# Optimization experiments

Measured on AMD Instinct MI355X. Metric: run time of the kernel, lower is better.

Reference implementation:

```python
import jax, jax.numpy as jnp
import numpy as np

D_MODEL = 1024
N_HEADS = 16
D_HEAD = D_MODEL // N_HEADS
FF = 4 * D_MODEL
B, S = 1, 2048
ROPE_BASE = 10000.0
LN_EPS = 1e-5


def setup_inputs() -> dict:
    key = jax.random.key(0)
    ks = jax.random.split(key, 12)
    sd = 0.02
    return {
        "x": jax.random.normal(ks[0], (B, S, D_MODEL), dtype=jnp.float32),
        # weights stored [in, out]
        "w_qkv": jax.random.normal(ks[1], (D_MODEL, 3 * D_MODEL), dtype=jnp.float32) * sd,
        "w_attn": jax.random.normal(ks[2], (D_MODEL, D_MODEL), dtype=jnp.float32) * sd,
        "b_attn": jnp.zeros((D_MODEL,), dtype=jnp.float32),
        "w_ff1": jax.random.normal(ks[3], (D_MODEL, FF), dtype=jnp.float32) * sd,
        "b_ff1": jnp.zeros((FF,), dtype=jnp.float32),
        "w_ff2": jax.random.normal(ks[4], (FF, D_MODEL), dtype=jnp.float32) * sd,
        "b_ff2": jnp.zeros((D_MODEL,), dtype=jnp.float32),
        "ln1_g": jnp.ones((D_MODEL,), dtype=jnp.float32),
        "ln1_b": jnp.zeros((D_MODEL,), dtype=jnp.float32),
        "ln2_g": jnp.ones((D_MODEL,), dtype=jnp.float32),
        "ln2_b": jnp.zeros((D_MODEL,), dtype=jnp.float32),
    }


def _layernorm(x, g, b):
    mu = jnp.mean(x, axis=-1, keepdims=True)
    var = jnp.mean(jnp.square(x - mu), axis=-1, keepdims=True)
    return (x - mu) * jax.lax.rsqrt(var + LN_EPS) * g + b


def _rope_cos_sin(seq_len, d_head, dtype):
    # scale=1.0 -> dynamic YaRN degenerates to vanilla RoPE with mscale=1
    inv_freq = 1.0 / (ROPE_BASE ** (jnp.arange(0, d_head, 2, dtype=jnp.float32) / d_head))
    pos = jnp.arange(seq_len, dtype=jnp.float32)
    freqs = pos[:, None] * inv_freq[None, :]          # [S, D/2]
    emb = jnp.concatenate([freqs, freqs], axis=-1)    # [S, D]
    return jnp.cos(emb).astype(dtype), jnp.sin(emb).astype(dtype)


def _rotate_half(x):
    x1, x2 = jnp.split(x, 2, axis=-1)
    return jnp.concatenate([-x2, x1], axis=-1)


def _apply_rope(q, k, cos, sin):
    # q,k: [B,S,H,D]; cos/sin: [S,D]
    c = cos[None, :, None, :]
    s = sin[None, :, None, :]
    return q * c + _rotate_half(q) * s, k * c + _rotate_half(k) * s


def _block(x, w_qkv, w_attn, b_attn, w_ff1, b_ff1, w_ff2, b_ff2,
           ln1_g, ln1_b, ln2_g, ln2_b):
    b, s, d = x.shape
    # --- attention sub-block (pre-norm) ---
    h = _layernorm(x, ln1_g, ln1_b)
    qkv = h @ w_qkv                                   # [B,S,3D]
    xq, xk, xv = jnp.split(qkv, 3, axis=-1)
    xq = xq.reshape(b, s, N_HEADS, D_HEAD)
    xk = xk.reshape(b, s, N_HEADS, D_HEAD)
    xv = xv.reshape(b, s, N_HEADS, D_HEAD)
    cos, sin = _rope_cos_sin(s, D_HEAD, x.dtype)
    xq, xk = _apply_rope(xq, xk, cos, sin)
    scale = 1.0 / np.sqrt(D_HEAD)
    scores = jnp.einsum("bqhd,bkhd->bhqk", xq, xk) * scale
    causal = jnp.tril(jnp.ones((s, s), dtype=bool))
    scores = jnp.where(causal[None, None], scores, jnp.finfo(scores.dtype).min)
    probs = jax.nn.softmax(scores, axis=-1)
    att = jnp.einsum("bhqk,bkhd->bqhd", probs, xv).reshape(b, s, d)
    x = x + (att @ w_attn + b_attn)
    # --- feed-forward sub-block (pre-norm) ---
    h2 = _layernorm(x, ln2_g, ln2_b)
    ff = jax.nn.gelu(h2 @ w_ff1 + b_ff1, approximate=False) @ w_ff2 + b_ff2
    return x + ff


def reference(x, w_qkv, w_attn, b_attn, w_ff1, b_ff1, w_ff2, b_ff2,
              ln1_g, ln1_b, ln2_g, ln2_b):
    return _block(x, w_qkv, w_attn, b_attn, w_ff1, b_ff1, w_ff2, b_ff2,
                  ln1_g, ln1_b, ln2_g, ln2_b)
```

## Files before the change

### kernel.cpp

```cpp
#include <hip/hip_runtime.h>
#include <hip/hip_bf16.h>
#include <stdint.h>

#define DM   1024
#define SEQ  2048
#define NH   16
#define DH   64
#define FFD  4096

typedef float  f32x4  __attribute__((ext_vector_type(4)));
typedef float  f32x16 __attribute__((ext_vector_type(16)));
typedef __bf16 bf16x8 __attribute__((ext_vector_type(8)));
typedef unsigned short u16;
typedef unsigned short u16x4v __attribute__((ext_vector_type(4)));
typedef unsigned short u16x8 __attribute__((ext_vector_type(8)));

__device__ __forceinline__ u16 f2bf(float f){
    unsigned int u = __builtin_bit_cast(unsigned int, f);
    u = u + 0x7FFFu + ((u >> 16) & 1u);
    return (u16)(u >> 16);
}
__device__ __forceinline__ float bf2f(u16 v){
    unsigned int u = ((unsigned int)v) << 16;
    return __builtin_bit_cast(float, u);
}
__device__ __forceinline__ f32x4 zero4(){ f32x4 v; v[0]=0.f;v[1]=0.f;v[2]=0.f;v[3]=0.f; return v; }
__device__ __forceinline__ unsigned int cvtpk(float lo, float hi){
    unsigned int r;
    asm("v_cvt_pk_bf16_f32 %0, %1, %2" : "=v"(r) : "v"(lo), "v"(hi));
    return r;
}

__device__ __forceinline__ void gload_lds16(const void* g, void* l){
    __builtin_amdgcn_global_load_lds(
        (const __attribute__((address_space(1))) unsigned int*)(uintptr_t)g,
        (__attribute__((address_space(3))) unsigned int*)(uintptr_t)l,
        16, 0, 0);
}

__global__ __launch_bounds__(256) void transall_k(const float* __restrict__ s0, u16* __restrict__ d0,
                                                  const float* __restrict__ s1, u16* __restrict__ d1,
                                                  const float* __restrict__ s2, u16* __restrict__ d2,
                                                  const float* __restrict__ s3, u16* __restrict__ d3){
    __shared__ float tile[64][65];
    const int b = blockIdx.x;
    const float* src; u16* dst; int K, N, bx, by;
    if (b < 768)      { src = s0; dst = d0; K = 1024; N = 3072; bx = b % 48;          by = b / 48; }
    else if (b < 1024){ src = s1; dst = d1; K = 1024; N = 1024; bx = (b-768) % 16;    by = (b-768) / 16; }
    else if (b < 2048){ src = s2; dst = d2; K = 1024; N = 4096; bx = (b-1024) % 64;   by = (b-1024) / 64; }
    else              { src = s3; dst = d3; K = 4096; N = 1024; bx = (b-2048) % 16;   by = (b-2048) / 16; }
    const int n0 = bx * 64, k0 = by * 64;
    const int t = threadIdx.x;
#pragma unroll
    for (int i = 0; i < 16; ++i){
        int idx = t + i * 256;
        int r = idx >> 6, c = idx & 63;
        tile[r][c] = src[(size_t)(k0 + r) * N + n0 + c];
    }
    __syncthreads();
#pragma unroll
    for (int i = 0; i < 16; ++i){
        int idx = t + i * 256;
        int r = idx >> 6, c = idx & 63;
        dst[(size_t)(n0 + r) * K + k0 + c] = f2bf(tile[c][r]);
    }
}

__global__ __launch_bounds__(256) void ln_k(const float* __restrict__ in,
                                            const float* __restrict__ gw,
                                            const float* __restrict__ bw,
                                            u16* __restrict__ out){
    const int row = blockIdx.x, t = threadIdx.x;
    f32x4 vv = *((const f32x4*)(in + (size_t)row * DM) + t);
    float v[4];
#pragma unroll
    for (int j = 0; j < 4; ++j) v[j] = vv[j];
    float s = 0.f, ss = 0.f;
#pragma unroll
    for (int j = 0; j < 4; ++j){ s += v[j]; ss += v[j] * v[j]; }
#pragma unroll
    for (int off = 1; off < 64; off <<= 1){
        s  += __shfl_xor(s,  off, 64);
        ss += __shfl_xor(ss, off, 64);
    }
    __shared__ float rs_[4], rss_[4];
    const int w = t >> 6;
    if ((t & 63) == 0){ rs_[w] = s; rss_[w] = ss; }
    __syncthreads();
    s  = rs_[0] + rs_[1] + rs_[2] + rs_[3];
    ss = rss_[0] + rss_[1] + rss_[2] + rss_[3];
    const float mean = s * (1.f / DM);
    const float var  = ss * (1.f / DM) - mean * mean;
    const float rstd = rsqrtf(var + 1e-5f);
#pragma unroll
    for (int j = 0; j < 4; ++j){
        int c = t * 4 + j;
        out[(size_t)row * DM + c] = f2bf((v[j] - mean) * rstd * gw[c] + bw[c]);
    }
}

template<int TM, int TN, int WR, int WC, int EPI>
__global__ __launch_bounds__(256) void gemm_k(const u16* __restrict__ A,
                                              const u16* __restrict__ Bt,
                                              const float* __restrict__ bias,
                                              const float* __restrict__ resid,
                                              void* __restrict__ out,
                                              u16* __restrict__ qout,
                                              u16* __restrict__ kout,
                                              u16* __restrict__ vout,
                                              int M, int N, int K){
    constexpr int MR   = TM / WR / 16;
    constexpr int NR   = TN / WC / 16;
    constexpr int AISS = (TM * 64) / 4096;
    constexpr int BISS = (TN * 64) / 4096;
    __shared__ u16 ldsAll[2 * TM * 32 + 2 * TN * 32];
    u16* ldsA = ldsAll;
    u16* ldsB = ldsAll + 2 * TM * 32;
    const int t = threadIdx.x;
    const int L = t & 63, w = t >> 6;
    const int g = L >> 4, li = L & 15;
    const int wr = w / WC, wc = w % WC;
    const int rowbase = wr * (TM / WR);
    const int colbase = wc * (TN / WC);
    const int nxb  = M / TM;
    const int nper = (int)gridDim.x >> 3;
    const int jswz = ((int)blockIdx.x & 7) * nper + ((int)blockIdx.x >> 3);
    const int brow = (jswz % nxb) * TM, bcol = (jswz / nxb) * TN;

    const u16* aPtr = A  + (size_t)brow * K;
    const u16* bPtr = Bt + (size_t)bcol * K;

    f32x4 acc[MR][NR];
#pragma unroll
    for (int m = 0; m < MR; ++m)
#pragma unroll
        for (int n = 0; n < NR; ++n) acc[m][n] = zero4();

    auto STAGE = [&](int buf, int ko){
#pragma unroll
        for (int i = 0; i < AISS; ++i){
            int o = i * 256 + t;
            gload_lds16(aPtr + (size_t)(o >> 2) * K + (o & 3) * 8 + ko, &ldsA[buf * TM * 32 + o * 8]);
        }
#pragma unroll
        for (int i = 0; i < BISS; ++i){
            int o = i * 256 + t;
            gload_lds16(bPtr + (size_t)(o >> 2) * K + (o & 3) * 8 + ko, &ldsB[buf * TN * 32 + o * 8]);
        }
    };

    const int KT = K >> 5;
    int cur = 0;
    STAGE(0, 0);
    __syncthreads();
    for (int kt = 0; kt < KT; ++kt){
        if (kt + 1 < KT) STAGE(cur ^ 1, (kt + 1) * 32);
        bf16x8 af[MR], bfr[NR];
#pragma unroll
        for (int m = 0; m < MR; ++m)
            af[m]  = *(const bf16x8*)&ldsA[cur * TM * 32 + (rowbase + m * 16 + li) * 32 + g * 8];
#pragma unroll
        for (int n = 0; n < NR; ++n)
            bfr[n] = *(const bf16x8*)&ldsB[cur * TN * 32 + (colbase + n * 16 + li) * 32 + g * 8];
#pragma unroll
        for (int m = 0; m < MR; ++m)
#pragma unroll
            for (int n = 0; n < NR; ++n)
                acc[m][n] = __builtin_amdgcn_mfma_f32_16x16x32_bf16(af[m], bfr[n], acc[m][n], 0, 0, 0);
        __syncthreads();
        cur ^= 1;
    }

    if constexpr (EPI == 4){
        const int colabs = bcol + colbase;
        const int part = colabs >> 10;
        if (part < 2){
            u16* dst = (part == 0) ? qout : kout;
            const int h = (colabs >> 6) & 15;
            float freq[2];
#pragma unroll
            for (int n = 0; n < 2; ++n)
                freq[n] = powf(10000.f, -(float)(n * 16 + li) * (1.f / 32.f));
#pragma unroll
            for (int m = 0; m < MR; ++m)
#pragma unroll
                for (int r = 0; r < 4; ++r){
                    const int srow = brow + rowbase + m * 16 + g * 4 + r;
                    const size_t tb = (size_t)(h * 64 + (srow >> 5)) * 2048
                                    + (li >> 3) * 256 + (srow & 31) * 8 + (li & 7);
#pragma unroll
                    for (int n = 0; n < 2; ++n){
                        float lo = acc[m][n][r], hi = acc[m][n + 2][r];
                        float sn, cs;
                        sincosf((float)srow * freq[n], &sn, &cs);
                        dst[tb + n * 512]       = f2bf(lo * cs - hi * sn);
                        dst[tb + (n + 2) * 512] = f2bf(hi * cs + lo * sn);
                    }
                }
        } else {
            u16* tileT = ldsAll;
            __syncthreads();
#pragma unroll
            for (int m = 0; m < MR; ++m)
#pragma unroll
                for (int n = 0; n < NR; ++n)
#pragma unroll
                    for (int r = 0; r < 4; ++r){
                        const int row = rowbase + m * 16 + g * 4 + r;
                        const int col = colbase + n * 16 + li;
                        tileT[col * 72 + row] = f2bf(acc[m][n][r]);
                    }
            __syncthreads();
            const int dv = t >> 1, half = t & 1;
            const int habs = ((bcol + dv) >> 6) & 15;
            const int dvl = dv & 63;
            const int f = dvl >> 5, dv5 = dvl & 31;
            const int tt = (brow >> 5) + half;
            u16* vbase = vout + (size_t)(habs * 64 + tt) * 2048 + f * 256 + dv5 * 8;
#pragma unroll
            for (int j = 0; j < 4; ++j)
                *(u16x8*)(vbase + (j >> 1) * 1024 + (j & 1) * 512)
                    = *(const u16x8*)&tileT[dv * 72 + half * 32 + j * 8];
        }
        return;
    }

#pragma unroll
    for (int m = 0; m < MR; ++m)
#pragma unroll
        for (int n = 0; n < NR; ++n)
#pragma unroll
            for (int r = 0; r < 4; ++r){
                const int row = brow + rowbase + m * 16 + g * 4 + r;
                const int col = bcol + colbase + n * 16 + li;
                float v = acc[m][n][r];
                if constexpr (EPI == 1){
                    v += bias[col] + resid[(size_t)row * N + col];
                    ((float*)out)[(size_t)row * N + col] = v;
                } else if constexpr (EPI == 2){
                    v += bias[col];
                    v = 0.5f * v * (1.f + erff(v * 0.70710678f));
                    ((u16*)out)[(size_t)row * N + col] = f2bf(v);
                } else {
                    v += bias[col] + resid[(size_t)row * N + col];
                    ((float*)out)[(size_t)row * N + col] = v;
                }
            }
}

#define CHT 8
__global__ __launch_bounds__(256) void attn_k(const u16* __restrict__ Qh,
                                              const u16* __restrict__ Kh,
                                              const u16* __restrict__ VT,
                                              u16* __restrict__ Opart,
                                              float* __restrict__ ml){
    const int t = threadIdx.x, w = t >> 6, L = t & 63;
    const int bid = blockIdx.x;
    const int xcd = bid & 7;
    const int lj  = (bid >> 3) * 4 + w;
    const int h   = xcd * 2 + (lj & 1);
    const int jd  = lj >> 1;
    int g = 7, rem = jd;
    while (rem >= 8 * (g + 1)){ rem -= 8 * (g + 1); --g; }
    const int gp1 = g + 1;
    const int qt = 8 * g + 7 - rem / gp1;
    const int c  = rem % gp1;
    const int t0 = c * CHT;
    const int tEnd = min(t0 + CHT, qt + 1);
    const int l31 = L & 31, H = L >> 5;

    const size_t hT = (size_t)h * 64;
    const int lane_off = H * 256 + l31 * 8;
    const int vlane_off = H * 512 + l31 * 8;

    const u16* qB = Qh + (hT + qt) * 2048 + lane_off;
    bf16x8 qf0 = *(const bf16x8*)(qB);
    bf16x8 qf1 = *(const bf16x8*)(qB + 512);
    bf16x8 qf2 = *(const bf16x8*)(qB + 1024);
    bf16x8 qf3 = *(const bf16x8*)(qB + 1536);

    const u16* kB0 = Kh + (hT + t0) * 2048 + lane_off;
    bf16x8 kc0 = *(const bf16x8*)(kB0);
    bf16x8 kc1 = *(const bf16x8*)(kB0 + 512);
    bf16x8 kc2 = *(const bf16x8*)(kB0 + 1024);
    bf16x8 kc3 = *(const bf16x8*)(kB0 + 1536);

    f32x16 O0, O1;
#pragma unroll
    for (int i = 0; i < 16; ++i){ O0[i] = 0.f; O1[i] = 0.f; }
    float m = -3.0e4f, lsum = 0.f;

    for (int tt = t0; tt < tEnd; ++tt){
        const u16* vB = VT + (hT + tt) * 2048 + vlane_off;
        bf16x8 v00 = *(const bf16x8*)(vB);
        bf16x8 v01 = *(const bf16x8*)(vB + 1024);
        bf16x8 v10 = *(const bf16x8*)(vB + 256);
        bf16x8 v11 = *(const bf16x8*)(vB + 1280);

        f32x16 st;
#pragma unroll
        for (int i = 0; i < 16; ++i) st[i] = 0.f;
        st = __builtin_amdgcn_mfma_f32_32x32x16_bf16(kc0, qf0, st, 0, 0, 0);
        st = __builtin_amdgcn_mfma_f32_32x32x16_bf16(kc1, qf1, st, 0, 0, 0);
        st = __builtin_amdgcn_mfma_f32_32x32x16_bf16(kc2, qf2, st, 0, 0, 0);
        st = __builtin_amdgcn_mfma_f32_32x32x16_bf16(kc3, qf3, st, 0, 0, 0);

        const bool more = (tt + 1 < tEnd);
        bf16x8 kn0, kn1, kn2, kn3;
        if (more){
            const u16* kBn = Kh + (hT + tt + 1) * 2048 + lane_off;
            kn0 = *(const bf16x8*)(kBn);
            kn1 = *(const bf16x8*)(kBn + 512);
            kn2 = *(const bf16x8*)(kBn + 1024);
            kn3 = *(const bf16x8*)(kBn + 1536);
        }

        const bool diag = (tt == qt);
        float sv[16];
#pragma unroll
        for (int i = 0; i < 16; ++i){
            float x = st[i] * 0.125f;
            if (diag){
                int kkl = (i & 3) + 8 * (i >> 2) + 4 * H;
                if (kkl > l31) x = -3.0e4f;
            }
            sv[i] = x;
        }
        float smax = sv[0];
#pragma unroll
        for (int i = 1; i < 16; ++i) smax = fmaxf(smax, sv[i]);
        smax = fmaxf(smax, __shfl_xor(smax, 32, 64));
        const float nm = fmaxf(m, smax);
        const float alpha = __expf(m - nm);
        m = nm;
        float ps = 0.f;
#pragma unroll
        for (int i = 0; i < 16; ++i){ sv[i] = __expf(sv[i] - m); ps += sv[i]; }
        ps += __shfl_xor(ps, 32, 64);
        lsum = lsum * alpha + ps;
#pragma unroll
        for (int i = 0; i < 16; ++i){ O0[i] *= alpha; O1[i] *= alpha; }

        unsigned int A0 = cvtpk(sv[0],  sv[1]),  A1 = cvtpk(sv[2],  sv[3]);
        unsigned int B0 = cvtpk(sv[4],  sv[5]),  B1 = cvtpk(sv[6],  sv[7]);
        unsigned int C0 = cvtpk(sv[8],  sv[9]),  C1 = cvtpk(sv[10], sv[11]);
        unsigned int D0 = cvtpk(sv[12], sv[13]), D1 = cvtpk(sv[14], sv[15]);
        unsigned int eA0 = (unsigned int)__shfl_xor((int)A0, 32, 64);
        unsigned int eA1 = (unsigned int)__shfl_xor((int)A1, 32, 64);
        unsigned int eB0 = (unsigned int)__shfl_xor((int)B0, 32, 64);
        unsigned int eB1 = (unsigned int)__shfl_xor((int)B1, 32, 64);
        unsigned int eC0 = (unsigned int)__shfl_xor((int)C0, 32, 64);
        unsigned int eC1 = (unsigned int)__shfl_xor((int)C1, 32, 64);
        unsigned int eD0 = (unsigned int)__shfl_xor((int)D0, 32, 64);
        unsigned int eD1 = (unsigned int)__shfl_xor((int)D1, 32, 64);
        union Uw { unsigned int w[4]; bf16x8 v; };
        Uw f0, f1;
        f0.w[0] = H ? eB0 : A0;  f0.w[1] = H ? eB1 : A1;
        f0.w[2] = H ? B0  : eA0; f0.w[3] = H ? B1  : eA1;
        f1.w[0] = H ? eD0 : C0;  f1.w[1] = H ? eD1 : C1;
        f1.w[2] = H ? D0  : eC0; f1.w[3] = H ? D1  : eC1;

        O0 = __builtin_amdgcn_mfma_f32_32x32x16_bf16(v00, f0.v, O0, 0, 0, 0);
        O0 = __builtin_amdgcn_mfma_f32_32x32x16_bf16(v01, f1.v, O0, 0, 0, 0);
        O1 = __builtin_amdgcn_mfma_f32_32x32x16_bf16(v10, f0.v, O1, 0, 0, 0);
        O1 = __builtin_amdgcn_mfma_f32_32x32x16_bf16(v11, f1.v, O1, 0, 0, 0);

        if (more){ kc0 = kn0; kc1 = kn1; kc2 = kn2; kc3 = kn3; }
    }

    const int jobd = h * 288 + jd;
    const size_t ob = (size_t)jobd * (32 * 64);
    const int q = l31;
#pragma unroll
    for (int f = 0; f < 2; ++f){
        const int dv0 = f * 32;
#pragma unroll
        for (int k = 0; k < 4; ++k){
            u16x4v pkv;
#pragma unroll
            for (int e = 0; e < 4; ++e)
                pkv[e] = f2bf(f == 0 ? O0[k * 4 + e] : O1[k * 4 + e]);
            *(u16x4v*)(Opart + ob + (size_t)q * 64 + dv0 + 8 * k + 4 * H) = pkv;
        }
    }
    if (H == 0){
        ml[((size_t)jobd * 32 + q) * 2]     = m;
        ml[((size_t)jobd * 32 + q) * 2 + 1] = lsum;
    }
}

__global__ __launch_bounds__(256) void combine_k(const u16* __restrict__ Opart,
                                                 const float* __restrict__ ml,
                                                 u16* __restrict__ att){
    const int qt = blockIdx.x, h = blockIdx.y;
    const int g = qt >> 3, gp1 = g + 1;
    const int off = 8 * (36 - ((gp1 * (g + 2)) >> 1));
    const int jd0 = off + (8 * g + 7 - qt) * gp1;
    const int j0 = h * 288 + jd0;
    const int nact = gp1;
    const int t = threadIdx.x;
    const int q = t >> 3, dv0 = (t & 7) * 8;

    float m = -3.0e30f;
    for (int cc = 0; cc < nact; ++cc)
        m = fmaxf(m, ml[((size_t)(j0 + cc) * 32 + q) * 2]);
    float Ls = 0.f;
    float o[8];
#pragma unroll
    for (int j = 0; j < 8; ++j) o[j] = 0.f;
    for (int cc = 0; cc < nact; ++cc){
        const float mv = ml[((size_t)(j0 + cc) * 32 + q) * 2];
        const float lv = ml[((size_t)(j0 + cc) * 32 + q) * 2 + 1];
        const float wgt = __expf(mv - m);
        Ls += wgt * lv;
        const u16* src = Opart + ((size_t)(j0 + cc) * 32 + q) * 64 + dv0;
        u16x8 a = *(const u16x8*)src;
#pragma unroll
        for (int e = 0; e < 8; ++e) o[e] += wgt * bf2f(a[e]);
    }
    const float inv = 1.f / Ls;
    const int qg = qt * 32 + q;
#pragma unroll
    for (int j = 0; j < 8; ++j)
        att[(size_t)qg * DM + h * 64 + dv0 + j] = f2bf(o[j] * inv);
}

extern "C" void kernel_launch(void* const* d_in, const int* in_sizes, int n_in,
                              void* d_out, int out_size, void* d_ws, size_t ws_size,
                              hipStream_t stream){
    (void)in_sizes; (void)n_in; (void)out_size; (void)ws_size;
    const float* x      = (const float*)d_in[0];
    const float* w_qkv  = (const float*)d_in[1];
    const float* w_attn = (const float*)d_in[2];
    const float* b_attn = (const float*)d_in[3];
    const float* w_ff1  = (const float*)d_in[4];
    const float* b_ff1  = (const float*)d_in[5];
    const float* w_ff2  = (const float*)d_in[6];
    const float* b_ff2  = (const float*)d_in[7];
    const float* ln1g   = (const float*)d_in[8];
    const float* ln1b   = (const float*)d_in[9];
    const float* ln2g   = (const float*)d_in[10];
    const float* ln2b   = (const float*)d_in[11];

    char* ws = (char*)d_ws;
    const size_t MB = 1u << 20;
    u16*   T1    = (u16*)(ws + 0);
    u16*   T2    = (u16*)(ws + 6  * MB);
    u16*   T3    = (u16*)(ws + 8  * MB);
    u16*   T4    = (u16*)(ws + 16 * MB);
    u16*   h1    = (u16*)(ws + 24 * MB);
    u16*   Qh    = (u16*)(ws + 28 * MB);
    u16*   Kh    = (u16*)(ws + 32 * MB);
    u16*   VT    = (u16*)(ws + 36 * MB);
    u16*   Opart = (u16*)(ws + 40 * MB);
    float* mlbuf = (float*)(ws + 59 * MB);
    u16*   att   = (u16*)(ws + 0);
    float* x2    = (float*)(ws + 40 * MB);
    u16*   h2    = (u16*)(ws + 4  * MB);
    u16*   ff    = (u16*)(ws + 24 * MB);

    transall_k<<<3072, 256, 0, stream>>>(w_qkv, T1, w_attn, T2, w_ff1, T3, w_ff2, T4);
    ln_k<<<SEQ, 256, 0, stream>>>(x, ln1g, ln1b, h1);
    gemm_k<64,128,2,2,4><<<768, 256, 0, stream>>>(h1, T1, nullptr, nullptr, nullptr,
                                                  Qh, Kh, VT, SEQ, 3072, 1024);
    attn_k<<<1152, 256, 0, stream>>>(Qh, Kh, VT, Opart, mlbuf);
    combine_k<<<dim3(64, 16), 256, 0, stream>>>(Opart, mlbuf, att);
    gemm_k<64,64,2,2,1><<<512, 256, 0, stream>>>(att, T2, b_attn, x, x2,
                                                 nullptr, nullptr, nullptr, SEQ, 1024, 1024);
    ln_k<<<SEQ, 256, 0, stream>>>(x2, ln2g, ln2b, h2);
    gemm_k<64,128,1,4,2><<<1024, 256, 0, stream>>>(h2, T3, b_ff1, nullptr, ff,
                                                   nullptr, nullptr, nullptr, SEQ, 4096, 1024);
    gemm_k<64,64,2,2,3><<<512, 256, 0, stream>>>(ff, T4, b_ff2, x2, (float*)d_out,
                                                 nullptr, nullptr, nullptr, SEQ, 1024, 4096);
}
```

Baseline: 178.4 us.

## Split-K the attention-output and FF2 GEMMs with a separate reduction kernel

Adds an NS split-K template parameter to the GEMM kernel. Each block computes a K-chunk and writes fp32 partials, and a new gcomb_k kernel sums them and adds the bias and residual. The attention-output GEMM uses 2 splits and the FF2 GEMM uses 4, which multiplies block counts to improve CU occupancy and shorten each block's long K loop. In exchange it adds extra global traffic for the partial buffers (up to 32 MB for FF2) and two extra kernel launches. It also assumes the workspace can hold the partials starting at 48 MB.

```diff
diff --git a/kernel.cpp b/kernel.cpp
--- a/kernel.cpp
+++ b/kernel.cpp
@@ -99,7 +99,7 @@
     }
 }
 
-template<int TM, int TN, int WR, int WC, int EPI>
+template<int TM, int TN, int WR, int WC, int EPI, int NS = 1>
 __global__ __launch_bounds__(256) void gemm_k(const u16* __restrict__ A,
                                               const u16* __restrict__ Bt,
                                               const float* __restrict__ bias,
@@ -123,12 +123,17 @@
     const int rowbase = wr * (TM / WR);
     const int colbase = wc * (TN / WC);
     const int nxb  = M / TM;
+    const int nyb  = N / TN;
     const int nper = (int)gridDim.x >> 3;
     const int jswz = ((int)blockIdx.x & 7) * nper + ((int)blockIdx.x >> 3);
-    const int brow = (jswz % nxb) * TM, bcol = (jswz / nxb) * TN;
-
-    const u16* aPtr = A  + (size_t)brow * K;
-    const u16* bPtr = Bt + (size_t)bcol * K;
+    int j2 = jswz, chunk = 0;
+    if (NS > 1){ chunk = j2 / (nxb * nyb); j2 -= chunk * (nxb * nyb); }
+    const int brow = (j2 % nxb) * TM, bcol = (j2 / nxb) * TN;
+    const int KC = K / NS;
+    const int kb = chunk * KC;
+
+    const u16* aPtr = A  + (size_t)brow * K + kb;
+    const u16* bPtr = Bt + (size_t)bcol * K + kb;
 
     f32x4 acc[MR][NR];
 #pragma unroll
@@ -149,7 +154,7 @@
         }
     };
 
-    const int KT = K >> 5;
+    const int KT = KC >> 5;
     int cur = 0;
     STAGE(0, 0);
     __syncthreads();
@@ -234,7 +239,9 @@
                 const int row = brow + rowbase + m * 16 + g * 4 + r;
                 const int col = bcol + colbase + n * 16 + li;
                 float v = acc[m][n][r];
-                if constexpr (EPI == 1){
+                if constexpr (NS > 1){
+                    ((float*)out)[((size_t)chunk * M + row) * N + col] = v;
+                } else if constexpr (EPI == 1){
                     v += bias[col] + resid[(size_t)row * N + col];
                     ((float*)out)[(size_t)row * N + col] = v;
                 } else if constexpr (EPI == 2){
@@ -246,6 +253,27 @@
                     ((float*)out)[(size_t)row * N + col] = v;
                 }
             }
+}
+
+template<int NS>
+__global__ __launch_bounds__(256) void gcomb_k(const float* __restrict__ P,
+                                               const float* __restrict__ bias,
+                                               const float* __restrict__ resid,
+                                               float* __restrict__ out){
+    const size_t base = ((size_t)blockIdx.x * 256 + threadIdx.x) * 4;
+    const int col = (int)(base & 1023);
+    f32x4 acc = *(const f32x4*)(P + base);
+#pragma unroll
+    for (int s = 1; s < NS; ++s){
+        f32x4 p = *(const f32x4*)(P + (size_t)s * (SEQ * 1024) + base);
+#pragma unroll
+        for (int e = 0; e < 4; ++e) acc[e] += p[e];
+    }
+    f32x4 b = *(const f32x4*)(bias + col);
+    f32x4 r = *(const f32x4*)(resid + base);
+#pragma unroll
+    for (int e = 0; e < 4; ++e) acc[e] += b[e] + r[e];
+    *(f32x4*)(out + base) = acc;
 }
 
 #define CHT 8
@@ -455,9 +483,11 @@
     u16*   Opart = (u16*)(ws + 40 * MB);
     float* mlbuf = (float*)(ws + 59 * MB);
     u16*   att   = (u16*)(ws + 0);
+    float* P1    = (float*)(ws + 48 * MB);
     float* x2    = (float*)(ws + 40 * MB);
     u16*   h2    = (u16*)(ws + 4  * MB);
     u16*   ff    = (u16*)(ws + 24 * MB);
+    float* P2    = (float*)(ws + 48 * MB);
 
     transall_k<<<3072, 256, 0, stream>>>(w_qkv, T1, w_attn, T2, w_ff1, T3, w_ff2, T4);
     ln_k<<<SEQ, 256, 0, stream>>>(x, ln1g, ln1b, h1);
@@ -465,11 +495,13 @@
                                                   Qh, Kh, VT, SEQ, 3072, 1024);
     attn_k<<<1152, 256, 0, stream>>>(Qh, Kh, VT, Opart, mlbuf);
     combine_k<<<dim3(64, 16), 256, 0, stream>>>(Opart, mlbuf, att);
-    gemm_k<64,64,2,2,1><<<512, 256, 0, stream>>>(att, T2, b_attn, x, x2,
-                                                 nullptr, nullptr, nullptr, SEQ, 1024, 1024);
+    gemm_k<64,64,2,2,1,2><<<1024, 256, 0, stream>>>(att, T2, nullptr, nullptr, P1,
+                                                    nullptr, nullptr, nullptr, SEQ, 1024, 1024);
+    gcomb_k<2><<<2048, 256, 0, stream>>>(P1, b_attn, x, x2);
     ln_k<<<SEQ, 256, 0, stream>>>(x2, ln2g, ln2b, h2);
     gemm_k<64,128,1,4,2><<<1024, 256, 0, stream>>>(h2, T3, b_ff1, nullptr, ff,
                                                    nullptr, nullptr, nullptr, SEQ, 4096, 1024);
-    gemm_k<64,64,2,2,3><<<512, 256, 0, stream>>>(ff, T4, b_ff2, x2, (float*)d_out,
-                                                 nullptr, nullptr, nullptr, SEQ, 1024, 4096);
-}
+    gemm_k<64,64,2,2,3,4><<<2048, 256, 0, stream>>>(ff, T4, nullptr, nullptr, P2,
+                                                    nullptr, nullptr, nullptr, SEQ, 1024, 4096);
+    gcomb_k<4><<<2048, 256, 0, stream>>>(P2, b_ff2, x2, (float*)d_out);
+}
```

Result: slower. 182.4 us (+2.3%).
